# Kernel tuning notes

Hardware: AMD Instinct MI355X
Metric: run time of the kernel (lower is better)

Reference implementation:

```python
import jax, jax.numpy as jnp
import numpy as np

N_NODES = 100000
N_EDGES = 1600000
DK = 32
OUT_DIM = 32


def setup_inputs() -> dict:
    key = jax.random.key(0)
    ks = jax.random.split(key, 7)
    X = jax.random.normal(ks[0], (N_NODES, DK), dtype=jnp.float32)
    K = jax.random.normal(ks[1], (N_NODES, DK), dtype=jnp.float32)
    V = jax.random.normal(ks[2], (N_NODES, DK), dtype=jnp.float32)
    # output projection (nn.Dense(out_dim)) params
    W_o = jax.random.normal(ks[3], (DK, OUT_DIM), dtype=jnp.float32) / np.sqrt(DK)
    b_o = jnp.zeros((OUT_DIM,), dtype=jnp.float32)
    # sparsity descriptor td: edge list, dst sorted so segment ops see sorted ids
    src = jax.random.randint(ks[4], (N_EDGES,), 0, N_NODES, dtype=jnp.int32)
    dst = jnp.sort(jax.random.randint(ks[5], (N_EDGES,), 0, N_NODES, dtype=jnp.int32))
    return {"X": X, "K": K, "V": V, "W_o": W_o, "b_o": b_o,
            "src": src, "dst": dst, "num_seg": N_NODES}


def reference(X, K, V, W_o, b_o, src, dst, num_seg):
    dk = X.shape[-1]
    # per-edge attention logits: <Q[dst], K[src]> / dk  -> (E,)
    scores = jnp.einsum('ed,ed->e', jnp.take(X, dst, axis=0),
                        jnp.take(K, src, axis=0)) / dk
    # segment (per-neighborhood) softmax over edges sharing a dst node
    seg_max = jax.ops.segment_max(scores, dst, num_segments=num_seg,
                                  indices_are_sorted=True)
    e = jnp.exp(scores - jnp.take(seg_max, dst))
    denom = jax.ops.segment_sum(e, dst, num_segments=num_seg,
                                indices_are_sorted=True)
    alpha = e / jnp.take(denom, dst)  # (E,)
    # weighted aggregation of values, scattered back to nodes -> (N, dk)
    agg = jax.ops.segment_sum(alpha[:, None] * jnp.take(V, src, axis=0), dst,
                              num_segments=num_seg, indices_are_sorted=True)
    # output projection W_o
    return agg @ W_o + b_o
```

## Files before the change

kernel.cpp:

```cpp
#include <hip/hip_runtime.h>
#include <math.h>

#define DK 32
#define OUT_DIM 32

typedef float  f32x4  __attribute__((ext_vector_type(4)));
typedef short  bf16x8 __attribute__((ext_vector_type(8)));

__global__ void build_row_ptr_kernel(const int* __restrict__ dst, int E, int N,
                                     int* __restrict__ row_ptr) {
    int e = blockIdx.x * blockDim.x + threadIdx.x;
    if (e >= E) return;
    int cur  = dst[e];
    int prev = (e == 0) ? -1 : dst[e - 1];
    for (int j = prev + 1; j <= cur; ++j) row_ptr[j] = e;
    if (e == E - 1) {
        for (int j = cur + 1; j <= N; ++j) row_ptr[j] = E;
    }
}

__device__ __forceinline__ unsigned f2bf_rne(float x) {
    unsigned u = __float_as_uint(x);
    return (u + 0x7fffu + ((u >> 16) & 1u)) >> 16;
}

__global__ void repack_kv_kernel(const float* __restrict__ K,
                                 const float* __restrict__ V,
                                 unsigned* __restrict__ KV, int total) {
    int i = blockIdx.x * blockDim.x + threadIdx.x;
    if (i >= total) return;
    KV[i] = (f2bf_rne(V[i]) << 16) | f2bf_rne(K[i]);
}

__global__ __launch_bounds__(256) void gat_fused_kernel(
    const float* __restrict__ X, const uint4* __restrict__ KV,
    const float* __restrict__ Wo, const float* __restrict__ bo,
    const int* __restrict__ src, const int* __restrict__ row_ptr,
    float* __restrict__ out, int N) {

    __shared__ uint4 s_part[4][16 * 17];

    const int tid  = threadIdx.x;
    const int wave = tid >> 6;
    const int lane = tid & 63;
    const int g    = lane >> 3;
    const int c    = lane & 7;
    const int quad = lane >> 4;
    const int col  = lane & 15;

    const int n0 = (blockIdx.x * 4 + wave) * 16;
    if (n0 >= N) return;

    union BF { bf16x8 v; unsigned short u[8]; };
    BF bf0, bf1;
#pragma unroll
    for (int j2 = 0; j2 < 8; ++j2) {
        bf0.u[j2] = (unsigned short)f2bf_rne(Wo[(quad * 8 + j2) * OUT_DIM + col]);
        bf1.u[j2] = (unsigned short)f2bf_rne(Wo[(quad * 8 + j2) * OUT_DIM + 16 + col]);
    }
    const float bias0 = bo[col];
    const float bias1 = bo[16 + col];

    const float4* X4 = (const float4*)X;
    unsigned* part32 = (unsigned*)&s_part[wave][0];

    for (int i = 0; i < 16; ++i) {
        const int n = n0 + i;
        float  l   = 0.0f;
        float4 acc = make_float4(0.0f, 0.0f, 0.0f, 0.0f);
        int begin = 0, end = 0;

        if (n < N) {
            begin = row_ptr[n];
            end   = row_ptr[n + 1];

            float4 q4 = X4[n * 8 + c];
            q4.x *= 0.03125f; q4.y *= 0.03125f;
            q4.z *= 0.03125f; q4.w *= 0.03125f;

            for (int e0 = begin; e0 < end; e0 += 16) {
                const int ea = e0 + g;
                const int eb = ea + 8;
                const int sa = src[min(ea, end - 1)];
                const int sb = src[min(eb, end - 1)];
                const uint4 A = KV[sa * 8 + c];
                const uint4 B = KV[sb * 8 + c];

                const float ka0 = __uint_as_float(A.x << 16);
                const float ka1 = __uint_as_float(A.y << 16);
                const float ka2 = __uint_as_float(A.z << 16);
                const float ka3 = __uint_as_float(A.w << 16);
                const float kb0 = __uint_as_float(B.x << 16);
                const float kb1 = __uint_as_float(B.y << 16);
                const float kb2 = __uint_as_float(B.z << 16);
                const float kb3 = __uint_as_float(B.w << 16);

                float pa = fmaf(ka0, q4.x, fmaf(ka1, q4.y, fmaf(ka2, q4.z, ka3 * q4.w)));
                float pb = fmaf(kb0, q4.x, fmaf(kb1, q4.y, fmaf(kb2, q4.z, kb3 * q4.w)));
                pa += __shfl_xor(pa, 1);  pb += __shfl_xor(pb, 1);
                pa += __shfl_xor(pa, 2);  pb += __shfl_xor(pb, 2);
                pa += __shfl_xor(pa, 4);  pb += __shfl_xor(pb, 4);

                const float wa = (ea < end) ? __expf(pa) : 0.0f;
                const float wb = (eb < end) ? __expf(pb) : 0.0f;
                l += wa + wb;

                acc.x = fmaf(wa, __uint_as_float(A.x & 0xffff0000u), acc.x);
                acc.y = fmaf(wa, __uint_as_float(A.y & 0xffff0000u), acc.y);
                acc.z = fmaf(wa, __uint_as_float(A.z & 0xffff0000u), acc.z);
                acc.w = fmaf(wa, __uint_as_float(A.w & 0xffff0000u), acc.w);
                acc.x = fmaf(wb, __uint_as_float(B.x & 0xffff0000u), acc.x);
                acc.y = fmaf(wb, __uint_as_float(B.y & 0xffff0000u), acc.y);
                acc.z = fmaf(wb, __uint_as_float(B.z & 0xffff0000u), acc.z);
                acc.w = fmaf(wb, __uint_as_float(B.w & 0xffff0000u), acc.w);
            }
        }

        l     += __shfl_xor(l, 8);
        acc.x += __shfl_xor(acc.x, 8);
        acc.y += __shfl_xor(acc.y, 8);
        acc.z += __shfl_xor(acc.z, 8);
        acc.w += __shfl_xor(acc.w, 8);
        l += __shfl_xor(l, 16);
        l += __shfl_xor(l, 32);

        const float inv = (end > begin) ? (1.0f / l) : 0.0f;
        acc.x *= inv; acc.y *= inv; acc.z *= inv; acc.w *= inv;

        if ((g & 1) == 0) {
            const int p   = g >> 1;
            const int off = i * 68 + p * 16 + c * 2;
            part32[off]     = f2bf_rne(acc.x) | (f2bf_rne(acc.y) << 16);
            part32[off + 1] = f2bf_rne(acc.z) | (f2bf_rne(acc.w) << 16);
        }
    }

    union AF { uint4 u; bf16x8 v; };
    f32x4 C0 = {bias0, bias0, bias0, bias0};
    f32x4 C1 = {bias1, bias1, bias1, bias1};
#pragma unroll
    for (int cc = 0; cc < 4; ++cc) {
        AF a;
        a.u = s_part[wave][col * 17 + cc * 4 + quad];
        C0 = __builtin_amdgcn_mfma_f32_16x16x32_bf16(a.v, bf0.v, C0, 0, 0, 0);
        C1 = __builtin_amdgcn_mfma_f32_16x16x32_bf16(a.v, bf1.v, C1, 0, 0, 0);
    }

#pragma unroll
    for (int r = 0; r < 4; ++r) {
        const int n = n0 + quad * 4 + r;
        if (n < N) {
            out[n * OUT_DIM + col]      = C0[r];
            out[n * OUT_DIM + 16 + col] = C1[r];
        }
    }
}

__global__ __launch_bounds__(256) void gat_node_f32_kernel(
    const float* __restrict__ X, const float* __restrict__ Km,
    const float* __restrict__ Vm, const float* __restrict__ Wo,
    const float* __restrict__ bo, const int* __restrict__ src,
    const int* __restrict__ row_ptr, float* __restrict__ out, int N) {
    const int tid  = threadIdx.x;
    const int wave = tid >> 6;
    const int lane = tid & 63;
    const int g    = lane >> 3;
    const int c    = lane & 7;
    const int j    = lane & 31;
    const int half = lane >> 5;
    const int n = blockIdx.x * 4 + wave;
    if (n >= N) return;
    const int begin = row_ptr[n];
    const int end   = row_ptr[n + 1];
    const float4* X4 = (const float4*)X;
    const float4* K4 = (const float4*)Km;
    const float4* V4 = (const float4*)Vm;
    const float4 q4 = X4[n * 8 + c];
    float  l   = 0.0f;
    float4 acc = make_float4(0.0f, 0.0f, 0.0f, 0.0f);
    for (int e0 = begin; e0 < end; e0 += 16) {
        const int  ea = e0 + g;
        const int  eb = ea + 8;
        const bool va = ea < end;
        const bool vb = eb < end;
        const int sa = src[min(ea, end - 1)];
        const int sb = src[min(eb, end - 1)];
        const float4 ka  = K4[sa * 8 + c];
        const float4 kb  = K4[sb * 8 + c];
        const float4 vva = V4[sa * 8 + c];
        const float4 vvb = V4[sb * 8 + c];
        float pa = fmaf(ka.x, q4.x, fmaf(ka.y, q4.y, fmaf(ka.z, q4.z, ka.w * q4.w)));
        float pb = fmaf(kb.x, q4.x, fmaf(kb.y, q4.y, fmaf(kb.z, q4.z, kb.w * q4.w)));
        pa += __shfl_xor(pa, 1);  pb += __shfl_xor(pb, 1);
        pa += __shfl_xor(pa, 2);  pb += __shfl_xor(pb, 2);
        pa += __shfl_xor(pa, 4);  pb += __shfl_xor(pb, 4);
        const float wa = va ? __expf(pa * 0.03125f) : 0.0f;
        const float wb = vb ? __expf(pb * 0.03125f) : 0.0f;
        l += wa + wb;
        acc.x = fmaf(wa, vva.x, acc.x);  acc.y = fmaf(wa, vva.y, acc.y);
        acc.z = fmaf(wa, vva.z, acc.z);  acc.w = fmaf(wa, vva.w, acc.w);
        acc.x = fmaf(wb, vvb.x, acc.x);  acc.y = fmaf(wb, vvb.y, acc.y);
        acc.z = fmaf(wb, vvb.z, acc.z);  acc.w = fmaf(wb, vvb.w, acc.w);
    }
#pragma unroll
    for (int m = 8; m <= 32; m <<= 1) {
        l     += __shfl_xor(l, m);
        acc.x += __shfl_xor(acc.x, m);
        acc.y += __shfl_xor(acc.y, m);
        acc.z += __shfl_xor(acc.z, m);
        acc.w += __shfl_xor(acc.w, m);
    }
    const float inv = (end > begin) ? (1.0f / l) : 0.0f;
    float ag[4] = {acc.x, acc.y, acc.z, acc.w};
    float s = 0.0f;
#pragma unroll
    for (int k = 0; k < 32; ++k) {
        const float a = __int_as_float(
            __builtin_amdgcn_readlane(__float_as_int(ag[k & 3]), k >> 2));
        s = fmaf(a, Wo[k * OUT_DIM + j], s);
    }
    if (half == 0) {
        out[n * OUT_DIM + j] = fmaf(s, inv, bo[j]);
    }
}

extern "C" void kernel_launch(void* const* d_in, const int* in_sizes, int n_in,
                              void* d_out, int out_size, void* d_ws, size_t ws_size,
                              hipStream_t stream) {
    const float* X  = (const float*)d_in[0];
    const float* Km = (const float*)d_in[1];
    const float* Vm = (const float*)d_in[2];
    const float* Wo = (const float*)d_in[3];
    const float* bo = (const float*)d_in[4];
    const int* src  = (const int*)d_in[5];
    const int* dst  = (const int*)d_in[6];

    const int N = in_sizes[0] / DK;
    const int E = in_sizes[5];

    int* row_ptr = (int*)d_ws;
    const size_t kv_off = (((size_t)(N + 1) * 4) + 127) & ~(size_t)127;
    unsigned* KV = (unsigned*)((char*)d_ws + kv_off);
    const size_t need = kv_off + (size_t)N * DK * 4;
    float* out = (float*)d_out;

    const int tb = 256;
    build_row_ptr_kernel<<<(E + tb - 1) / tb, tb, 0, stream>>>(dst, E, N, row_ptr);

    if (ws_size >= need) {
        const int total = N * DK;
        repack_kv_kernel<<<(total + tb - 1) / tb, tb, 0, stream>>>(Km, Vm, KV, total);
        const int waves = (N + 15) / 16;
        const int grid  = (waves + 3) / 4;
        gat_fused_kernel<<<grid, 256, 0, stream>>>(X, (const uint4*)KV, Wo, bo,
                                                   src, row_ptr, out, N);
    } else {
        const int grid = (N + 3) / 4;
        gat_node_f32_kernel<<<grid, 256, 0, stream>>>(X, Km, Vm, Wo, bo,
                                                      src, row_ptr, out, N);
    }
}
```

Baseline: 151.9 us.

## Merge prep kernels and process two nodes per iteration with readlane row pointers

Merges the row-pointer build and the K/V bf16 repack into one prep kernel, which drops a kernel launch. In the main kernel, each wave loads its 17 row_ptr entries once into a register and reads them with readlane instead of doing per-node scalar loads. It then processes two destination nodes at once, interleaving their gathers so more memory loads are in flight. This costs more registers and divergent branches when the two nodes have different degrees.

```diff
diff --git a/kernel.cpp b/kernel.cpp
--- a/kernel.cpp
+++ b/kernel.cpp
@@ -6,6 +6,31 @@
 
 typedef float  f32x4  __attribute__((ext_vector_type(4)));
 typedef short  bf16x8 __attribute__((ext_vector_type(8)));
+
+__device__ __forceinline__ unsigned f2bf_rne(float x) {
+    unsigned u = __float_as_uint(x);
+    return (u + 0x7fffu + ((u >> 16) & 1u)) >> 16;
+}
+
+__global__ void prep_kernel(const int* __restrict__ dst,
+                            const float* __restrict__ K,
+                            const float* __restrict__ V,
+                            int E, int N,
+                            int* __restrict__ row_ptr,
+                            unsigned* __restrict__ KV) {
+    const int t = blockIdx.x * blockDim.x + threadIdx.x;
+    if (t < E) {
+        const int cur  = dst[t];
+        const int prev = (t == 0) ? -1 : dst[t - 1];
+        for (int j = prev + 1; j <= cur; ++j) row_ptr[j] = t;
+        if (t == E - 1) {
+            for (int j = cur + 1; j <= N; ++j) row_ptr[j] = E;
+        }
+    }
+    if (t < N * DK) {
+        KV[t] = (f2bf_rne(V[t]) << 16) | f2bf_rne(K[t]);
+    }
+}
 
 __global__ void build_row_ptr_kernel(const int* __restrict__ dst, int E, int N,
                                      int* __restrict__ row_ptr) {
@@ -19,19 +44,6 @@
     }
 }
 
-__device__ __forceinline__ unsigned f2bf_rne(float x) {
-    unsigned u = __float_as_uint(x);
-    return (u + 0x7fffu + ((u >> 16) & 1u)) >> 16;
-}
-
-__global__ void repack_kv_kernel(const float* __restrict__ K,
-                                 const float* __restrict__ V,
-                                 unsigned* __restrict__ KV, int total) {
-    int i = blockIdx.x * blockDim.x + threadIdx.x;
-    if (i >= total) return;
-    KV[i] = (f2bf_rne(V[i]) << 16) | f2bf_rne(K[i]);
-}
-
 __global__ __launch_bounds__(256) void gat_fused_kernel(
     const float* __restrict__ X, const uint4* __restrict__ KV,
     const float* __restrict__ Wo, const float* __restrict__ bo,
@@ -61,77 +73,119 @@
     const float bias0 = bo[col];
     const float bias1 = bo[16 + col];
 
+    const int rp_reg = row_ptr[min(n0 + min(lane, 16), N)];
+
     const float4* X4 = (const float4*)X;
     unsigned* part32 = (unsigned*)&s_part[wave][0];
-
-    for (int i = 0; i < 16; ++i) {
-        const int n = n0 + i;
-        float  l   = 0.0f;
-        float4 acc = make_float4(0.0f, 0.0f, 0.0f, 0.0f);
-        int begin = 0, end = 0;
-
-        if (n < N) {
-            begin = row_ptr[n];
-            end   = row_ptr[n + 1];
-
-            float4 q4 = X4[n * 8 + c];
-            q4.x *= 0.03125f; q4.y *= 0.03125f;
-            q4.z *= 0.03125f; q4.w *= 0.03125f;
-
-            for (int e0 = begin; e0 < end; e0 += 16) {
-                const int ea = e0 + g;
-                const int eb = ea + 8;
-                const int sa = src[min(ea, end - 1)];
-                const int sb = src[min(eb, end - 1)];
-                const uint4 A = KV[sa * 8 + c];
-                const uint4 B = KV[sb * 8 + c];
-
-                const float ka0 = __uint_as_float(A.x << 16);
-                const float ka1 = __uint_as_float(A.y << 16);
-                const float ka2 = __uint_as_float(A.z << 16);
-                const float ka3 = __uint_as_float(A.w << 16);
-                const float kb0 = __uint_as_float(B.x << 16);
-                const float kb1 = __uint_as_float(B.y << 16);
-                const float kb2 = __uint_as_float(B.z << 16);
-                const float kb3 = __uint_as_float(B.w << 16);
-
-                float pa = fmaf(ka0, q4.x, fmaf(ka1, q4.y, fmaf(ka2, q4.z, ka3 * q4.w)));
-                float pb = fmaf(kb0, q4.x, fmaf(kb1, q4.y, fmaf(kb2, q4.z, kb3 * q4.w)));
-                pa += __shfl_xor(pa, 1);  pb += __shfl_xor(pb, 1);
-                pa += __shfl_xor(pa, 2);  pb += __shfl_xor(pb, 2);
-                pa += __shfl_xor(pa, 4);  pb += __shfl_xor(pb, 4);
-
-                const float wa = (ea < end) ? __expf(pa) : 0.0f;
-                const float wb = (eb < end) ? __expf(pb) : 0.0f;
-                l += wa + wb;
-
-                acc.x = fmaf(wa, __uint_as_float(A.x & 0xffff0000u), acc.x);
-                acc.y = fmaf(wa, __uint_as_float(A.y & 0xffff0000u), acc.y);
-                acc.z = fmaf(wa, __uint_as_float(A.z & 0xffff0000u), acc.z);
-                acc.w = fmaf(wa, __uint_as_float(A.w & 0xffff0000u), acc.w);
-                acc.x = fmaf(wb, __uint_as_float(B.x & 0xffff0000u), acc.x);
-                acc.y = fmaf(wb, __uint_as_float(B.y & 0xffff0000u), acc.y);
-                acc.z = fmaf(wb, __uint_as_float(B.z & 0xffff0000u), acc.z);
-                acc.w = fmaf(wb, __uint_as_float(B.w & 0xffff0000u), acc.w);
+    const float scale = 0.03125f;
+
+    for (int i = 0; i < 16; i += 2) {
+        const int beginA = __builtin_amdgcn_readlane(rp_reg, i);
+        const int mid    = __builtin_amdgcn_readlane(rp_reg, i + 1);
+        const int endB   = __builtin_amdgcn_readlane(rp_reg, i + 2);
+        const int endA   = mid, beginB = mid;
+        const int nA = n0 + i, nB = n0 + i + 1;
+
+        float4 qA = X4[min(nA, N - 1) * 8 + c];
+        float4 qB = X4[min(nB, N - 1) * 8 + c];
+        qA.x *= scale; qA.y *= scale; qA.z *= scale; qA.w *= scale;
+        qB.x *= scale; qB.y *= scale; qB.z *= scale; qB.w *= scale;
+
+        float  lA = 0.0f, lB = 0.0f;
+        float4 aA = make_float4(0.f, 0.f, 0.f, 0.f);
+        float4 aB = make_float4(0.f, 0.f, 0.f, 0.f);
+
+        int eA = beginA, eB = beginB;
+        while (eA < endA || eB < endB) {
+            const bool actA = eA < endA;
+            const bool actB = eB < endB;
+            int s0 = 0, s1 = 0, s2 = 0, s3 = 0;
+            uint4 A0, A1, B0, B1;
+            if (actA) {
+                s0 = src[min(eA + g,     endA - 1)];
+                s1 = src[min(eA + 8 + g, endA - 1)];
             }
+            if (actB) {
+                s2 = src[min(eB + g,     endB - 1)];
+                s3 = src[min(eB + 8 + g, endB - 1)];
+            }
+            if (actA) { A0 = KV[s0 * 8 + c]; A1 = KV[s1 * 8 + c]; }
+            if (actB) { B0 = KV[s2 * 8 + c]; B1 = KV[s3 * 8 + c]; }
+
+            if (actA) {
+                float p0 = fmaf(__uint_as_float(A0.x << 16), qA.x,
+                           fmaf(__uint_as_float(A0.y << 16), qA.y,
+                           fmaf(__uint_as_float(A0.z << 16), qA.z,
+                                __uint_as_float(A0.w << 16) * qA.w)));
+                float p1 = fmaf(__uint_as_float(A1.x << 16), qA.x,
+                           fmaf(__uint_as_float(A1.y << 16), qA.y,
+                           fmaf(__uint_as_float(A1.z << 16), qA.z,
+                                __uint_as_float(A1.w << 16) * qA.w)));
+                p0 += __shfl_xor(p0, 1);  p1 += __shfl_xor(p1, 1);
+                p0 += __shfl_xor(p0, 2);  p1 += __shfl_xor(p1, 2);
+                p0 += __shfl_xor(p0, 4);  p1 += __shfl_xor(p1, 4);
+                const float w0 = (eA + g     < endA) ? __expf(p0) : 0.0f;
+                const float w1 = (eA + 8 + g < endA) ? __expf(p1) : 0.0f;
+                lA += w0 + w1;
+                aA.x = fmaf(w0, __uint_as_float(A0.x & 0xffff0000u), aA.x);
+                aA.y = fmaf(w0, __uint_as_float(A0.y & 0xffff0000u), aA.y);
+                aA.z = fmaf(w0, __uint_as_float(A0.z & 0xffff0000u), aA.z);
+                aA.w = fmaf(w0, __uint_as_float(A0.w & 0xffff0000u), aA.w);
+                aA.x = fmaf(w1, __uint_as_float(A1.x & 0xffff0000u), aA.x);
+                aA.y = fmaf(w1, __uint_as_float(A1.y & 0xffff0000u), aA.y);
+                aA.z = fmaf(w1, __uint_as_float(A1.z & 0xffff0000u), aA.z);
+                aA.w = fmaf(w1, __uint_as_float(A1.w & 0xffff0000u), aA.w);
+            }
+            if (actB) {
+                float p2 = fmaf(__uint_as_float(B0.x << 16), qB.x,
+                           fmaf(__uint_as_float(B0.y << 16), qB.y,
+                           fmaf(__uint_as_float(B0.z << 16), qB.z,
+                                __uint_as_float(B0.w << 16) * qB.w)));
+                float p3 = fmaf(__uint_as_float(B1.x << 16), qB.x,
+                           fmaf(__uint_as_float(B1.y << 16), qB.y,
+                           fmaf(__uint_as_float(B1.z << 16), qB.z,
+                                __uint_as_float(B1.w << 16) * qB.w)));
+                p2 += __shfl_xor(p2, 1);  p3 += __shfl_xor(p3, 1);
+                p2 += __shfl_xor(p2, 2);  p3 += __shfl_xor(p3, 2);
+                p2 += __shfl_xor(p2, 4);  p3 += __shfl_xor(p3, 4);
+                const float w2 = (eB + g     < endB) ? __expf(p2) : 0.0f;
+                const float w3 = (eB + 8 + g < endB) ? __expf(p3) : 0.0f;
+                lB += w2 + w3;
+                aB.x = fmaf(w2, __uint_as_float(B0.x & 0xffff0000u), aB.x);
+                aB.y = fmaf(w2, __uint_as_float(B0.y & 0xffff0000u), aB.y);
+                aB.z = fmaf(w2, __uint_as_float(B0.z & 0xffff0000u), aB.z);
+                aB.w = fmaf(w2, __uint_as_float(B0.w & 0xffff0000u), aB.w);
+                aB.x = fmaf(w3, __uint_as_float(B1.x & 0xffff0000u), aB.x);
+                aB.y = fmaf(w3, __uint_as_float(B1.y & 0xffff0000u), aB.y);
+                aB.z = fmaf(w3, __uint_as_float(B1.z & 0xffff0000u), aB.z);
+                aB.w = fmaf(w3, __uint_as_float(B1.w & 0xffff0000u), aB.w);
+            }
+            eA += 16; eB += 16;
         }
 
-        l     += __shfl_xor(l, 8);
-        acc.x += __shfl_xor(acc.x, 8);
-        acc.y += __shfl_xor(acc.y, 8);
-        acc.z += __shfl_xor(acc.z, 8);
-        acc.w += __shfl_xor(acc.w, 8);
-        l += __shfl_xor(l, 16);
-        l += __shfl_xor(l, 32);
-
-        const float inv = (end > begin) ? (1.0f / l) : 0.0f;
-        acc.x *= inv; acc.y *= inv; acc.z *= inv; acc.w *= inv;
+        lA   += __shfl_xor(lA, 8);
+        aA.x += __shfl_xor(aA.x, 8);  aA.y += __shfl_xor(aA.y, 8);
+        aA.z += __shfl_xor(aA.z, 8);  aA.w += __shfl_xor(aA.w, 8);
+        lA += __shfl_xor(lA, 16);  lA += __shfl_xor(lA, 32);
+
+        lB   += __shfl_xor(lB, 8);
+        aB.x += __shfl_xor(aB.x, 8);  aB.y += __shfl_xor(aB.y, 8);
+        aB.z += __shfl_xor(aB.z, 8);  aB.w += __shfl_xor(aB.w, 8);
+        lB += __shfl_xor(lB, 16);  lB += __shfl_xor(lB, 32);
+
+        const float invA = (endA > beginA) ? (1.0f / lA) : 0.0f;
+        const float invB = (endB > beginB) ? (1.0f / lB) : 0.0f;
+        aA.x *= invA; aA.y *= invA; aA.z *= invA; aA.w *= invA;
+        aB.x *= invB; aB.y *= invB; aB.z *= invB; aB.w *= invB;
 
         if ((g & 1) == 0) {
-            const int p   = g >> 1;
-            const int off = i * 68 + p * 16 + c * 2;
-            part32[off]     = f2bf_rne(acc.x) | (f2bf_rne(acc.y) << 16);
-            part32[off + 1] = f2bf_rne(acc.z) | (f2bf_rne(acc.w) << 16);
+            const int p = g >> 1;
+            int off = i * 68 + p * 16 + c * 2;
+            part32[off]     = f2bf_rne(aA.x) | (f2bf_rne(aA.y) << 16);
+            part32[off + 1] = f2bf_rne(aA.z) | (f2bf_rne(aA.w) << 16);
+            off += 68;
+            part32[off]     = f2bf_rne(aB.x) | (f2bf_rne(aB.y) << 16);
+            part32[off + 1] = f2bf_rne(aB.z) | (f2bf_rne(aB.w) << 16);
         }
     }
 
@@ -245,16 +299,18 @@
     float* out = (float*)d_out;
 
     const int tb = 256;
-    build_row_ptr_kernel<<<(E + tb - 1) / tb, tb, 0, stream>>>(dst, E, N, row_ptr);
 
     if (ws_size >= need) {
-        const int total = N * DK;
-        repack_kv_kernel<<<(total + tb - 1) / tb, tb, 0, stream>>>(Km, Vm, KV, total);
+        const int total   = N * DK;
+        const int prep_n  = (E > total) ? E : total;
+        prep_kernel<<<(prep_n + tb - 1) / tb, tb, 0, stream>>>(dst, Km, Vm, E, N,
+                                                               row_ptr, KV);
         const int waves = (N + 15) / 16;
         const int grid  = (waves + 3) / 4;
         gat_fused_kernel<<<grid, 256, 0, stream>>>(X, (const uint4*)KV, Wo, bo,
                                                    src, row_ptr, out, N);
     } else {
+        build_row_ptr_kernel<<<(E + tb - 1) / tb, tb, 0, stream>>>(dst, E, N, row_ptr);
         const int grid = (N + 3) / 4;
         gat_node_f32_kernel<<<grid, 256, 0, stream>>>(X, Km, Vm, Wo, bo,
                                                       src, row_ptr, out, N);
```

After: 162.9 us. +7.2%, slower.

## Merge prep kernels, stage src in LDS, and software-pipeline edge gathers

Applied to the files above, without the earlier changes.

Row-pointer building and K/V bf16 repacking now run in one prep kernel, which saves a launch. In the fused kernel each wave first copies the src indices for its 16 nodes into shared memory, up to 512 of them. It then walks those edges as one continuous stream and prefetches the next chunk's KV rows and query while it computes the current chunk, so gather latency overlaps with compute across node boundaries. Waves with more than 512 edges fall back to the old per-node loop. The cost is extra LDS use (about 8KB per block) and a __syncthreads, which could lower occupancy.

```diff
diff --git a/kernel.cpp b/kernel.cpp
--- a/kernel.cpp
+++ b/kernel.cpp
@@ -3,9 +3,35 @@
 
 #define DK 32
 #define OUT_DIM 32
+#define SRC_CAP 512
 
 typedef float  f32x4  __attribute__((ext_vector_type(4)));
 typedef short  bf16x8 __attribute__((ext_vector_type(8)));
+
+__device__ __forceinline__ unsigned f2bf_rne(float x) {
+    unsigned u = __float_as_uint(x);
+    return (u + 0x7fffu + ((u >> 16) & 1u)) >> 16;
+}
+
+__global__ void prep_kernel(const int* __restrict__ dst,
+                            const float* __restrict__ K,
+                            const float* __restrict__ V,
+                            int E, int N,
+                            int* __restrict__ row_ptr,
+                            unsigned* __restrict__ KV) {
+    const int t = blockIdx.x * blockDim.x + threadIdx.x;
+    if (t < E) {
+        const int cur  = dst[t];
+        const int prev = (t == 0) ? -1 : dst[t - 1];
+        for (int j = prev + 1; j <= cur; ++j) row_ptr[j] = t;
+        if (t == E - 1) {
+            for (int j = cur + 1; j <= N; ++j) row_ptr[j] = E;
+        }
+    }
+    if (t < N * DK) {
+        KV[t] = (f2bf_rne(V[t]) << 16) | f2bf_rne(K[t]);
+    }
+}
 
 __global__ void build_row_ptr_kernel(const int* __restrict__ dst, int E, int N,
                                      int* __restrict__ row_ptr) {
@@ -19,19 +45,6 @@
     }
 }
 
-__device__ __forceinline__ unsigned f2bf_rne(float x) {
-    unsigned u = __float_as_uint(x);
-    return (u + 0x7fffu + ((u >> 16) & 1u)) >> 16;
-}
-
-__global__ void repack_kv_kernel(const float* __restrict__ K,
-                                 const float* __restrict__ V,
-                                 unsigned* __restrict__ KV, int total) {
-    int i = blockIdx.x * blockDim.x + threadIdx.x;
-    if (i >= total) return;
-    KV[i] = (f2bf_rne(V[i]) << 16) | f2bf_rne(K[i]);
-}
-
 __global__ __launch_bounds__(256) void gat_fused_kernel(
     const float* __restrict__ X, const uint4* __restrict__ KV,
     const float* __restrict__ Wo, const float* __restrict__ bo,
@@ -39,6 +52,8 @@
     float* __restrict__ out, int N) {
 
     __shared__ uint4 s_part[4][16 * 17];
+    __shared__ int   s_src[4][SRC_CAP];
+    __shared__ int   s_rp[4][17];
 
     const int tid  = threadIdx.x;
     const int wave = tid >> 6;
@@ -49,6 +64,22 @@
     const int col  = lane & 15;
 
     const int n0 = (blockIdx.x * 4 + wave) * 16;
+
+    const int rpv = row_ptr[min(n0 + min(lane, 16), N)];
+    if (lane <= 16) s_rp[wave][lane] = rpv;
+    const int Bv    = __shfl(rpv, 0);
+    const int Endv  = __shfl(rpv, 16);
+    const int count = Endv - Bv;
+
+    int* srcbuf = s_src[wave];
+    if (count > 0 && count <= SRC_CAP) {
+        const int iters = (count + 63) >> 6;
+        for (int k = 0; k < iters; ++k) {
+            const int idx = (k << 6) + lane;
+            srcbuf[idx] = src[Bv + min(idx, count - 1)];
+        }
+    }
+    __syncthreads();
     if (n0 >= N) return;
 
     union BF { bf16x8 v; unsigned short u[8]; };
@@ -63,75 +94,149 @@
 
     const float4* X4 = (const float4*)X;
     unsigned* part32 = (unsigned*)&s_part[wave][0];
-
-    for (int i = 0; i < 16; ++i) {
-        const int n = n0 + i;
+    const int* rp    = s_rp[wave];
+    const float scale = 0.03125f;
+
+    if (count == 0) {
+        const uint4 z = make_uint4(0u, 0u, 0u, 0u);
+        for (int t = lane; t < 16 * 17; t += 64) s_part[wave][t] = z;
+    } else if (count <= SRC_CAP) {
+        int i   = 0;
+        int end = rp[1];
+        int e   = Bv;
+
+        float4 q = X4[min(n0, N - 1) * 8 + c];
+        q.x *= scale; q.y *= scale; q.z *= scale; q.w *= scale;
+
+        int i0 = min(e + g,     Endv - 1) - Bv;
+        int i1 = min(e + 8 + g, Endv - 1) - Bv;
+        int s0 = srcbuf[i0];
+        int s1 = srcbuf[i1];
+        uint4 A0 = KV[s0 * 8 + c];
+        uint4 A1 = KV[s1 * 8 + c];
+
         float  l   = 0.0f;
-        float4 acc = make_float4(0.0f, 0.0f, 0.0f, 0.0f);
-        int begin = 0, end = 0;
-
-        if (n < N) {
-            begin = row_ptr[n];
-            end   = row_ptr[n + 1];
-
-            float4 q4 = X4[n * 8 + c];
-            q4.x *= 0.03125f; q4.y *= 0.03125f;
-            q4.z *= 0.03125f; q4.w *= 0.03125f;
-
-            for (int e0 = begin; e0 < end; e0 += 16) {
-                const int ea = e0 + g;
-                const int eb = ea + 8;
-                const int sa = src[min(ea, end - 1)];
-                const int sb = src[min(eb, end - 1)];
+        float4 acc = make_float4(0.f, 0.f, 0.f, 0.f);
+
+        while (true) {
+            const bool last = (e + 16 >= end);
+            const int  e2   = last ? end : (e + 16);
+            const int  end2 = last ? rp[min(i + 2, 16)] : end;
+
+            const int j0 = min(e2 + g,     Endv - 1) - Bv;
+            const int j1 = min(e2 + 8 + g, Endv - 1) - Bv;
+            const int t0 = srcbuf[j0];
+            const int t1 = srcbuf[j1];
+            const uint4 P0 = KV[t0 * 8 + c];
+            const uint4 P1 = KV[t1 * 8 + c];
+
+            float4 qn = q;
+            if (last) {
+                qn = X4[min(n0 + i + 1, N - 1) * 8 + c];
+                qn.x *= scale; qn.y *= scale; qn.z *= scale; qn.w *= scale;
+            }
+
+            float p0 = fmaf(__uint_as_float(A0.x << 16), q.x,
+                       fmaf(__uint_as_float(A0.y << 16), q.y,
+                       fmaf(__uint_as_float(A0.z << 16), q.z,
+                            __uint_as_float(A0.w << 16) * q.w)));
+            float p1 = fmaf(__uint_as_float(A1.x << 16), q.x,
+                       fmaf(__uint_as_float(A1.y << 16), q.y,
+                       fmaf(__uint_as_float(A1.z << 16), q.z,
+                            __uint_as_float(A1.w << 16) * q.w)));
+            p0 += __shfl_xor(p0, 1);  p1 += __shfl_xor(p1, 1);
+            p0 += __shfl_xor(p0, 2);  p1 += __shfl_xor(p1, 2);
+            p0 += __shfl_xor(p0, 4);  p1 += __shfl_xor(p1, 4);
+
+            const float w0 = (e + g     < end) ? __expf(p0) : 0.0f;
+            const float w1 = (e + 8 + g < end) ? __expf(p1) : 0.0f;
+            l += w0 + w1;
+
+            acc.x = fmaf(w0, __uint_as_float(A0.x & 0xffff0000u), acc.x);
+            acc.y = fmaf(w0, __uint_as_float(A0.y & 0xffff0000u), acc.y);
+            acc.z = fmaf(w0, __uint_as_float(A0.z & 0xffff0000u), acc.z);
+            acc.w = fmaf(w0, __uint_as_float(A0.w & 0xffff0000u), acc.w);
+            acc.x = fmaf(w1, __uint_as_float(A1.x & 0xffff0000u), acc.x);
+            acc.y = fmaf(w1, __uint_as_float(A1.y & 0xffff0000u), acc.y);
+            acc.z = fmaf(w1, __uint_as_float(A1.z & 0xffff0000u), acc.z);
+            acc.w = fmaf(w1, __uint_as_float(A1.w & 0xffff0000u), acc.w);
+
+            if (last) {
+                l     += __shfl_xor(l, 8);
+                acc.x += __shfl_xor(acc.x, 8);  acc.y += __shfl_xor(acc.y, 8);
+                acc.z += __shfl_xor(acc.z, 8);  acc.w += __shfl_xor(acc.w, 8);
+                l += __shfl_xor(l, 16);  l += __shfl_xor(l, 32);
+
+                const float inv = (l > 0.0f) ? (1.0f / l) : 0.0f;
+                acc.x *= inv; acc.y *= inv; acc.z *= inv; acc.w *= inv;
+
+                if ((g & 1) == 0) {
+                    const int p   = g >> 1;
+                    const int off = i * 68 + p * 16 + c * 2;
+                    part32[off]     = f2bf_rne(acc.x) | (f2bf_rne(acc.y) << 16);
+                    part32[off + 1] = f2bf_rne(acc.z) | (f2bf_rne(acc.w) << 16);
+                }
+                l = 0.0f;
+                acc = make_float4(0.f, 0.f, 0.f, 0.f);
+                ++i;
+                if (i >= 16) break;
+            }
+            e = e2; end = end2;
+            A0 = P0; A1 = P1; q = qn;
+        }
+    } else {
+        for (int i = 0; i < 16; ++i) {
+            const int begin = rp[i];
+            const int endn  = rp[i + 1];
+            float4 q = X4[min(n0 + i, N - 1) * 8 + c];
+            q.x *= scale; q.y *= scale; q.z *= scale; q.w *= scale;
+
+            float  l   = 0.0f;
+            float4 acc = make_float4(0.f, 0.f, 0.f, 0.f);
+
+            for (int e0 = begin; e0 < endn; e0 += 16) {
+                const int sa = src[min(e0 + g,     endn - 1)];
+                const int sb = src[min(e0 + 8 + g, endn - 1)];
                 const uint4 A = KV[sa * 8 + c];
                 const uint4 B = KV[sb * 8 + c];
-
-                const float ka0 = __uint_as_float(A.x << 16);
-                const float ka1 = __uint_as_float(A.y << 16);
-                const float ka2 = __uint_as_float(A.z << 16);
-                const float ka3 = __uint_as_float(A.w << 16);
-                const float kb0 = __uint_as_float(B.x << 16);
-                const float kb1 = __uint_as_float(B.y << 16);
-                const float kb2 = __uint_as_float(B.z << 16);
-                const float kb3 = __uint_as_float(B.w << 16);
-
-                float pa = fmaf(ka0, q4.x, fmaf(ka1, q4.y, fmaf(ka2, q4.z, ka3 * q4.w)));
-                float pb = fmaf(kb0, q4.x, fmaf(kb1, q4.y, fmaf(kb2, q4.z, kb3 * q4.w)));
-                pa += __shfl_xor(pa, 1);  pb += __shfl_xor(pb, 1);
-                pa += __shfl_xor(pa, 2);  pb += __shfl_xor(pb, 2);
-                pa += __shfl_xor(pa, 4);  pb += __shfl_xor(pb, 4);
-
-                const float wa = (ea < end) ? __expf(pa) : 0.0f;
-                const float wb = (eb < end) ? __expf(pb) : 0.0f;
-                l += wa + wb;
-
-                acc.x = fmaf(wa, __uint_as_float(A.x & 0xffff0000u), acc.x);
-                acc.y = fmaf(wa, __uint_as_float(A.y & 0xffff0000u), acc.y);
-                acc.z = fmaf(wa, __uint_as_float(A.z & 0xffff0000u), acc.z);
-                acc.w = fmaf(wa, __uint_as_float(A.w & 0xffff0000u), acc.w);
-                acc.x = fmaf(wb, __uint_as_float(B.x & 0xffff0000u), acc.x);
-                acc.y = fmaf(wb, __uint_as_float(B.y & 0xffff0000u), acc.y);
-                acc.z = fmaf(wb, __uint_as_float(B.z & 0xffff0000u), acc.z);
-                acc.w = fmaf(wb, __uint_as_float(B.w & 0xffff0000u), acc.w);
+                float p0 = fmaf(__uint_as_float(A.x << 16), q.x,
+                           fmaf(__uint_as_float(A.y << 16), q.y,
+                           fmaf(__uint_as_float(A.z << 16), q.z,
+                                __uint_as_float(A.w << 16) * q.w)));
+                float p1 = fmaf(__uint_as_float(B.x << 16), q.x,
+                           fmaf(__uint_as_float(B.y << 16), q.y,
+                           fmaf(__uint_as_float(B.z << 16), q.z,
+                                __uint_as_float(B.w << 16) * q.w)));
+                p0 += __shfl_xor(p0, 1);  p1 += __shfl_xor(p1, 1);
+                p0 += __shfl_xor(p0, 2);  p1 += __shfl_xor(p1, 2);
+                p0 += __shfl_xor(p0, 4);  p1 += __shfl_xor(p1, 4);
+                const float w0 = (e0 + g     < endn) ? __expf(p0) : 0.0f;
+                const float w1 = (e0 + 8 + g < endn) ? __expf(p1) : 0.0f;
+                l += w0 + w1;
+                acc.x = fmaf(w0, __uint_as_float(A.x & 0xffff0000u), acc.x);
+                acc.y = fmaf(w0, __uint_as_float(A.y & 0xffff0000u), acc.y);
+                acc.z = fmaf(w0, __uint_as_float(A.z & 0xffff0000u), acc.z);
+                acc.w = fmaf(w0, __uint_as_float(A.w & 0xffff0000u), acc.w);
+                acc.x = fmaf(w1, __uint_as_float(B.x & 0xffff0000u), acc.x);
+                acc.y = fmaf(w1, __uint_as_float(B.y & 0xffff0000u), acc.y);
+                acc.z = fmaf(w1, __uint_as_float(B.z & 0xffff0000u), acc.z);
+                acc.w = fmaf(w1, __uint_as_float(B.w & 0xffff0000u), acc.w);
             }
-        }
-
-        l     += __shfl_xor(l, 8);
-        acc.x += __shfl_xor(acc.x, 8);
-        acc.y += __shfl_xor(acc.y, 8);
-        acc.z += __shfl_xor(acc.z, 8);
-        acc.w += __shfl_xor(acc.w, 8);
-        l += __shfl_xor(l, 16);
-        l += __shfl_xor(l, 32);
-
-        const float inv = (end > begin) ? (1.0f / l) : 0.0f;
-        acc.x *= inv; acc.y *= inv; acc.z *= inv; acc.w *= inv;
-
-        if ((g & 1) == 0) {
-            const int p   = g >> 1;
-            const int off = i * 68 + p * 16 + c * 2;
-            part32[off]     = f2bf_rne(acc.x) | (f2bf_rne(acc.y) << 16);
-            part32[off + 1] = f2bf_rne(acc.z) | (f2bf_rne(acc.w) << 16);
+
+            l     += __shfl_xor(l, 8);
+            acc.x += __shfl_xor(acc.x, 8);  acc.y += __shfl_xor(acc.y, 8);
+            acc.z += __shfl_xor(acc.z, 8);  acc.w += __shfl_xor(acc.w, 8);
+            l += __shfl_xor(l, 16);  l += __shfl_xor(l, 32);
+
+            const float inv = (l > 0.0f) ? (1.0f / l) : 0.0f;
+            acc.x *= inv; acc.y *= inv; acc.z *= inv; acc.w *= inv;
+
+            if ((g & 1) == 0) {
+                const int p   = g >> 1;
+                const int off = i * 68 + p * 16 + c * 2;
+                part32[off]     = f2bf_rne(acc.x) | (f2bf_rne(acc.y) << 16);
+                part32[off + 1] = f2bf_rne(acc.z) | (f2bf_rne(acc.w) << 16);
+            }
         }
     }
 
@@ -145,7 +250,6 @@
         C0 = __builtin_amdgcn_mfma_f32_16x16x32_bf16(a.v, bf0.v, C0, 0, 0, 0);
         C1 = __builtin_amdgcn_mfma_f32_16x16x32_bf16(a.v, bf1.v, C1, 0, 0, 0);
     }
-
 #pragma unroll
     for (int r = 0; r < 4; ++r) {
         const int n = n0 + quad * 4 + r;
@@ -245,16 +349,18 @@
     float* out = (float*)d_out;
 
     const int tb = 256;
-    build_row_ptr_kernel<<<(E + tb - 1) / tb, tb, 0, stream>>>(dst, E, N, row_ptr);
 
     if (ws_size >= need) {
-        const int total = N * DK;
-        repack_kv_kernel<<<(total + tb - 1) / tb, tb, 0, stream>>>(Km, Vm, KV, total);
+        const int total  = N * DK;
+        const int prep_n = (E > total) ? E : total;
+        prep_kernel<<<(prep_n + tb - 1) / tb, tb, 0, stream>>>(dst, Km, Vm, E, N,
+                                                               row_ptr, KV);
         const int waves = (N + 15) / 16;
         const int grid  = (waves + 3) / 4;
         gat_fused_kernel<<<grid, 256, 0, stream>>>(X, (const uint4*)KV, Wo, bo,
                                                    src, row_ptr, out, N);
     } else {
+        build_row_ptr_kernel<<<(E + tb - 1) / tb, tb, 0, stream>>>(dst, E, N, row_ptr);
         const int grid = (N + 3) / 4;
         gat_node_f32_kernel<<<grid, 256, 0, stream>>>(X, Km, Vm, Wo, bo,
                                                       src, row_ptr, out, N);
```

New measurement: 149.2 us. No clear change (-1.8%).

## Merge prep kernels and spread 16-node tiles across four waves per block

Applied to the files above, without the earlier changes.

Combines row-pointer construction and the K/V bf16 repack into one prep launch, removing a kernel launch. The fused kernel now assigns 16 nodes per block (4 per wave instead of 16), which gives 4x more blocks and shorter serial per-wave loops. Row pointers are loaded once per wave and broadcast via readlane. A block barrier then lets wave 0 alone run the MFMA output projection, so the other three waves idle during that step.

```diff
diff --git a/kernel.cpp b/kernel.cpp
--- a/kernel.cpp
+++ b/kernel.cpp
@@ -6,6 +6,31 @@
 
 typedef float  f32x4  __attribute__((ext_vector_type(4)));
 typedef short  bf16x8 __attribute__((ext_vector_type(8)));
+
+__device__ __forceinline__ unsigned f2bf_rne(float x) {
+    unsigned u = __float_as_uint(x);
+    return (u + 0x7fffu + ((u >> 16) & 1u)) >> 16;
+}
+
+__global__ void prep_kernel(const int* __restrict__ dst,
+                            const float* __restrict__ K,
+                            const float* __restrict__ V,
+                            int E, int N,
+                            int* __restrict__ row_ptr,
+                            unsigned* __restrict__ KV) {
+    const int t = blockIdx.x * blockDim.x + threadIdx.x;
+    if (t < E) {
+        const int cur  = dst[t];
+        const int prev = (t == 0) ? -1 : dst[t - 1];
+        for (int j = prev + 1; j <= cur; ++j) row_ptr[j] = t;
+        if (t == E - 1) {
+            for (int j = cur + 1; j <= N; ++j) row_ptr[j] = E;
+        }
+    }
+    if (t < N * DK) {
+        KV[t] = (f2bf_rne(V[t]) << 16) | f2bf_rne(K[t]);
+    }
+}
 
 __global__ void build_row_ptr_kernel(const int* __restrict__ dst, int E, int N,
                                      int* __restrict__ row_ptr) {
@@ -19,139 +44,122 @@
     }
 }
 
-__device__ __forceinline__ unsigned f2bf_rne(float x) {
-    unsigned u = __float_as_uint(x);
-    return (u + 0x7fffu + ((u >> 16) & 1u)) >> 16;
-}
-
-__global__ void repack_kv_kernel(const float* __restrict__ K,
-                                 const float* __restrict__ V,
-                                 unsigned* __restrict__ KV, int total) {
-    int i = blockIdx.x * blockDim.x + threadIdx.x;
-    if (i >= total) return;
-    KV[i] = (f2bf_rne(V[i]) << 16) | f2bf_rne(K[i]);
-}
-
 __global__ __launch_bounds__(256) void gat_fused_kernel(
     const float* __restrict__ X, const uint4* __restrict__ KV,
     const float* __restrict__ Wo, const float* __restrict__ bo,
     const int* __restrict__ src, const int* __restrict__ row_ptr,
     float* __restrict__ out, int N) {
 
-    __shared__ uint4 s_part[4][16 * 17];
+    __shared__ uint4 s_part[16 * 17];
 
     const int tid  = threadIdx.x;
-    const int wave = tid >> 6;
+    const int w    = tid >> 6;
     const int lane = tid & 63;
     const int g    = lane >> 3;
     const int c    = lane & 7;
-    const int quad = lane >> 4;
-    const int col  = lane & 15;
-
-    const int n0 = (blockIdx.x * 4 + wave) * 16;
-    if (n0 >= N) return;
-
-    union BF { bf16x8 v; unsigned short u[8]; };
-    BF bf0, bf1;
-#pragma unroll
-    for (int j2 = 0; j2 < 8; ++j2) {
-        bf0.u[j2] = (unsigned short)f2bf_rne(Wo[(quad * 8 + j2) * OUT_DIM + col]);
-        bf1.u[j2] = (unsigned short)f2bf_rne(Wo[(quad * 8 + j2) * OUT_DIM + 16 + col]);
-    }
-    const float bias0 = bo[col];
-    const float bias1 = bo[16 + col];
+
+    const int n_blk = blockIdx.x * 16;
+    const int n_w   = n_blk + w * 4;
+
+    const int rpv = row_ptr[min(n_w + min(lane, 4), N)];
 
     const float4* X4 = (const float4*)X;
-    unsigned* part32 = (unsigned*)&s_part[wave][0];
-
-    for (int i = 0; i < 16; ++i) {
-        const int n = n0 + i;
+    unsigned* part32 = (unsigned*)s_part;
+    const float scale = 0.03125f;
+
+    for (int i = 0; i < 4; ++i) {
+        const int begin = __builtin_amdgcn_readlane(rpv, i);
+        const int end   = __builtin_amdgcn_readlane(rpv, i + 1);
+        const int n     = n_w + i;
+
+        float4 q = X4[min(n, N - 1) * 8 + c];
+        q.x *= scale; q.y *= scale; q.z *= scale; q.w *= scale;
+
         float  l   = 0.0f;
-        float4 acc = make_float4(0.0f, 0.0f, 0.0f, 0.0f);
-        int begin = 0, end = 0;
-
-        if (n < N) {
-            begin = row_ptr[n];
-            end   = row_ptr[n + 1];
-
-            float4 q4 = X4[n * 8 + c];
-            q4.x *= 0.03125f; q4.y *= 0.03125f;
-            q4.z *= 0.03125f; q4.w *= 0.03125f;
-
-            for (int e0 = begin; e0 < end; e0 += 16) {
-                const int ea = e0 + g;
-                const int eb = ea + 8;
-                const int sa = src[min(ea, end - 1)];
-                const int sb = src[min(eb, end - 1)];
-                const uint4 A = KV[sa * 8 + c];
-                const uint4 B = KV[sb * 8 + c];
-
-                const float ka0 = __uint_as_float(A.x << 16);
-                const float ka1 = __uint_as_float(A.y << 16);
-                const float ka2 = __uint_as_float(A.z << 16);
-                const float ka3 = __uint_as_float(A.w << 16);
-                const float kb0 = __uint_as_float(B.x << 16);
-                const float kb1 = __uint_as_float(B.y << 16);
-                const float kb2 = __uint_as_float(B.z << 16);
-                const float kb3 = __uint_as_float(B.w << 16);
-
-                float pa = fmaf(ka0, q4.x, fmaf(ka1, q4.y, fmaf(ka2, q4.z, ka3 * q4.w)));
-                float pb = fmaf(kb0, q4.x, fmaf(kb1, q4.y, fmaf(kb2, q4.z, kb3 * q4.w)));
-                pa += __shfl_xor(pa, 1);  pb += __shfl_xor(pb, 1);
-                pa += __shfl_xor(pa, 2);  pb += __shfl_xor(pb, 2);
-                pa += __shfl_xor(pa, 4);  pb += __shfl_xor(pb, 4);
-
-                const float wa = (ea < end) ? __expf(pa) : 0.0f;
-                const float wb = (eb < end) ? __expf(pb) : 0.0f;
-                l += wa + wb;
-
-                acc.x = fmaf(wa, __uint_as_float(A.x & 0xffff0000u), acc.x);
-                acc.y = fmaf(wa, __uint_as_float(A.y & 0xffff0000u), acc.y);
-                acc.z = fmaf(wa, __uint_as_float(A.z & 0xffff0000u), acc.z);
-                acc.w = fmaf(wa, __uint_as_float(A.w & 0xffff0000u), acc.w);
-                acc.x = fmaf(wb, __uint_as_float(B.x & 0xffff0000u), acc.x);
-                acc.y = fmaf(wb, __uint_as_float(B.y & 0xffff0000u), acc.y);
-                acc.z = fmaf(wb, __uint_as_float(B.z & 0xffff0000u), acc.z);
-                acc.w = fmaf(wb, __uint_as_float(B.w & 0xffff0000u), acc.w);
-            }
+        float4 acc = make_float4(0.f, 0.f, 0.f, 0.f);
+
+        for (int e0 = begin; e0 < end; e0 += 16) {
+            const int sa = src[min(e0 + g,     end - 1)];
+            const int sb = src[min(e0 + 8 + g, end - 1)];
+            const uint4 A = KV[sa * 8 + c];
+            const uint4 B = KV[sb * 8 + c];
+
+            float p0 = fmaf(__uint_as_float(A.x << 16), q.x,
+                       fmaf(__uint_as_float(A.y << 16), q.y,
+                       fmaf(__uint_as_float(A.z << 16), q.z,
+                            __uint_as_float(A.w << 16) * q.w)));
+            float p1 = fmaf(__uint_as_float(B.x << 16), q.x,
+                       fmaf(__uint_as_float(B.y << 16), q.y,
+                       fmaf(__uint_as_float(B.z << 16), q.z,
+                            __uint_as_float(B.w << 16) * q.w)));
+            p0 += __shfl_xor(p0, 1);  p1 += __shfl_xor(p1, 1);
+            p0 += __shfl_xor(p0, 2);  p1 += __shfl_xor(p1, 2);
+            p0 += __shfl_xor(p0, 4);  p1 += __shfl_xor(p1, 4);
+
+            const float w0 = (e0 + g     < end) ? __expf(p0) : 0.0f;
+            const float w1 = (e0 + 8 + g < end) ? __expf(p1) : 0.0f;
+            l += w0 + w1;
+
+            acc.x = fmaf(w0, __uint_as_float(A.x & 0xffff0000u), acc.x);
+            acc.y = fmaf(w0, __uint_as_float(A.y & 0xffff0000u), acc.y);
+            acc.z = fmaf(w0, __uint_as_float(A.z & 0xffff0000u), acc.z);
+            acc.w = fmaf(w0, __uint_as_float(A.w & 0xffff0000u), acc.w);
+            acc.x = fmaf(w1, __uint_as_float(B.x & 0xffff0000u), acc.x);
+            acc.y = fmaf(w1, __uint_as_float(B.y & 0xffff0000u), acc.y);
+            acc.z = fmaf(w1, __uint_as_float(B.z & 0xffff0000u), acc.z);
+            acc.w = fmaf(w1, __uint_as_float(B.w & 0xffff0000u), acc.w);
         }
 
         l     += __shfl_xor(l, 8);
-        acc.x += __shfl_xor(acc.x, 8);
-        acc.y += __shfl_xor(acc.y, 8);
-        acc.z += __shfl_xor(acc.z, 8);
-        acc.w += __shfl_xor(acc.w, 8);
-        l += __shfl_xor(l, 16);
-        l += __shfl_xor(l, 32);
+        acc.x += __shfl_xor(acc.x, 8);  acc.y += __shfl_xor(acc.y, 8);
+        acc.z += __shfl_xor(acc.z, 8);  acc.w += __shfl_xor(acc.w, 8);
+        l += __shfl_xor(l, 16);  l += __shfl_xor(l, 32);
 
         const float inv = (end > begin) ? (1.0f / l) : 0.0f;
         acc.x *= inv; acc.y *= inv; acc.z *= inv; acc.w *= inv;
 
         if ((g & 1) == 0) {
             const int p   = g >> 1;
-            const int off = i * 68 + p * 16 + c * 2;
+            const int row = w * 4 + i;
+            const int off = row * 68 + p * 16 + c * 2;
             part32[off]     = f2bf_rne(acc.x) | (f2bf_rne(acc.y) << 16);
             part32[off + 1] = f2bf_rne(acc.z) | (f2bf_rne(acc.w) << 16);
         }
     }
 
-    union AF { uint4 u; bf16x8 v; };
-    f32x4 C0 = {bias0, bias0, bias0, bias0};
-    f32x4 C1 = {bias1, bias1, bias1, bias1};
-#pragma unroll
-    for (int cc = 0; cc < 4; ++cc) {
-        AF a;
-        a.u = s_part[wave][col * 17 + cc * 4 + quad];
-        C0 = __builtin_amdgcn_mfma_f32_16x16x32_bf16(a.v, bf0.v, C0, 0, 0, 0);
-        C1 = __builtin_amdgcn_mfma_f32_16x16x32_bf16(a.v, bf1.v, C1, 0, 0, 0);
-    }
-
-#pragma unroll
-    for (int r = 0; r < 4; ++r) {
-        const int n = n0 + quad * 4 + r;
-        if (n < N) {
-            out[n * OUT_DIM + col]      = C0[r];
-            out[n * OUT_DIM + 16 + col] = C1[r];
+    __syncthreads();
+
+    if (w == 0) {
+        const int quad = lane >> 4;
+        const int col  = lane & 15;
+
+        union BF { bf16x8 v; unsigned short u[8]; };
+        BF bf0, bf1;
+#pragma unroll
+        for (int j2 = 0; j2 < 8; ++j2) {
+            bf0.u[j2] = (unsigned short)f2bf_rne(Wo[(quad * 8 + j2) * OUT_DIM + col]);
+            bf1.u[j2] = (unsigned short)f2bf_rne(Wo[(quad * 8 + j2) * OUT_DIM + 16 + col]);
+        }
+        const float bias0 = bo[col];
+        const float bias1 = bo[16 + col];
+
+        union AF { uint4 u; bf16x8 v; };
+        f32x4 C0 = {bias0, bias0, bias0, bias0};
+        f32x4 C1 = {bias1, bias1, bias1, bias1};
+#pragma unroll
+        for (int cc = 0; cc < 4; ++cc) {
+            AF a;
+            a.u = s_part[col * 17 + cc * 4 + quad];
+            C0 = __builtin_amdgcn_mfma_f32_16x16x32_bf16(a.v, bf0.v, C0, 0, 0, 0);
+            C1 = __builtin_amdgcn_mfma_f32_16x16x32_bf16(a.v, bf1.v, C1, 0, 0, 0);
+        }
+#pragma unroll
+        for (int r = 0; r < 4; ++r) {
+            const int n = n_blk + quad * 4 + r;
+            if (n < N) {
+                out[n * OUT_DIM + col]      = C0[r];
+                out[n * OUT_DIM + 16 + col] = C1[r];
+            }
         }
     }
 }
@@ -245,16 +253,17 @@
     float* out = (float*)d_out;
 
     const int tb = 256;
-    build_row_ptr_kernel<<<(E + tb - 1) / tb, tb, 0, stream>>>(dst, E, N, row_ptr);
 
     if (ws_size >= need) {
-        const int total = N * DK;
-        repack_kv_kernel<<<(total + tb - 1) / tb, tb, 0, stream>>>(Km, Vm, KV, total);
-        const int waves = (N + 15) / 16;
-        const int grid  = (waves + 3) / 4;
+        const int total  = N * DK;
+        const int prep_n = (E > total) ? E : total;
+        prep_kernel<<<(prep_n + tb - 1) / tb, tb, 0, stream>>>(dst, Km, Vm, E, N,
+                                                               row_ptr, KV);
+        const int grid = (N + 15) / 16;
         gat_fused_kernel<<<grid, 256, 0, stream>>>(X, (const uint4*)KV, Wo, bo,
                                                    src, row_ptr, out, N);
     } else {
+        build_row_ptr_kernel<<<(E + tb - 1) / tb, tb, 0, stream>>>(dst, E, N, row_ptr);
         const int grid = (N + 3) / 4;
         gat_node_f32_kernel<<<grid, 256, 0, stream>>>(X, Km, Vm, Wo, bo,
                                                       src, row_ptr, out, N);
```

Result: faster. 140.8 us (-7.3%).
